# Kernel optimization log

Hardware: AMD Instinct MI355X
Metric: run time of the kernel (lower is better)

The kernel has to match this reference:

```python
import jax, jax.numpy as jnp
import numpy as np
import math

B, S, D, H = 8, 1024, 512, 8
DH = D // H
SCALE_BASE = 512


def _xpos(x, downscale):
    # x: [B, H, S, DH]; xpos rotary with exponential scale (jamie-stirling RetNet impl)
    s = x.shape[-2]
    d = x.shape[-1]
    half = d // 2
    sv = (jnp.arange(0, d, 2, dtype=jnp.float32) + 0.4 * d) / (1.4 * d)      # [half]
    power = jnp.arange(s, dtype=jnp.float32) / SCALE_BASE
    scale = sv[None, :] ** power[:, None]                                     # [s, half]
    inv_freq = 1.0 / (10000.0 ** (jnp.arange(half, dtype=jnp.float32) / half))
    ang = jnp.arange(s, dtype=jnp.float32)[:, None] * inv_freq[None, :]       # [s, half]
    if downscale:
        scale = 1.0 / scale
    sin = jnp.repeat(jnp.sin(ang) * scale, 2, axis=-1)                        # [s, d]
    cos = jnp.repeat(jnp.cos(ang) * scale, 2, axis=-1)
    rot = jnp.stack((-x[..., 1::2], x[..., ::2]), axis=-1).reshape(x.shape)   # rotate_every_two
    return x * cos + rot * sin


def setup_inputs() -> dict:
    key = jax.random.key(0)
    ks = jax.random.split(key, 7)
    X = jax.random.normal(ks[0], (B, S, D), dtype=jnp.float32)
    # per-head projections stacked: torch init randn/hidden_size
    W_Q = jax.random.normal(ks[1], (H, D, DH), dtype=jnp.float32) / D
    W_K = jax.random.normal(ks[2], (H, D, DH), dtype=jnp.float32) / D
    W_V = jax.random.normal(ks[3], (H, D, DH), dtype=jnp.float32) / D
    W_G = jax.random.normal(ks[4], (D, D), dtype=jnp.float32) / D
    W_O = jax.random.normal(ks[5], (D, D), dtype=jnp.float32) / D
    gn_weight = jnp.ones((D,), dtype=jnp.float32)
    gn_bias = jnp.zeros((D,), dtype=jnp.float32)
    return {"X": X, "W_Q": W_Q, "W_K": W_K, "W_V": W_V, "W_G": W_G,
            "W_O": W_O, "gn_weight": gn_weight, "gn_bias": gn_bias}


def reference(X, W_Q, W_K, W_V, W_G, W_O, gn_weight, gn_bias):
    b, s, _ = X.shape
    # per-head decay gammas and symmetric (non-causal) decay matrix D
    gammas = 1.0 - jnp.exp(jnp.linspace(math.log(1.0 / 32), math.log(1.0 / 512), H)).astype(jnp.float32)
    n = jnp.arange(s)
    Dmat = gammas[:, None, None] ** jnp.abs(n[:, None] - n[None, :]).astype(jnp.float32)  # [H,s,s]
    Q = _xpos(jnp.einsum('bsd,hde->bhse', X, W_Q), False)
    K = _xpos(jnp.einsum('bsd,hde->bhse', X, W_K), True)
    V = jnp.einsum('bsd,hde->bhse', X, W_V)
    scores = jnp.einsum('bhse,bhte->bhst', Q, K)
    p = jax.nn.softmax(scores, axis=-1) * Dmat[None]          # decay-weighted softmax
    Y = jnp.einsum('bhst,bhte->bhse', p, V)                    # [b,H,s,DH]
    Y = jnp.moveaxis(Y, 1, 2).reshape(b, s, H * DH)            # concat heads -> [b,s,D]
    # GroupNorm(H groups) over flattened rows [b*s, D]
    Yg = Y.reshape(-1, H, DH)
    mu = Yg.mean(axis=-1, keepdims=True)
    var = Yg.var(axis=-1, keepdims=True)
    Yn = ((Yg - mu) * jax.lax.rsqrt(var + 1e-5)).reshape(-1, H * DH)
    Yn = (Yn * gn_weight + gn_bias).reshape(b, s, H * DH)
    G = X @ W_G
    swish = G * jax.nn.sigmoid(G)
    return (swish * Yn) @ W_O
```

## Files before the change

### kernel.cpp

```cpp
#include <hip/hip_runtime.h>
#include <math.h>

#define B_ 8
#define S_ 1024
#define D_ 512
#define H_ 8
#define DH_ 64
#define M_ (B_*S_)

typedef __attribute__((ext_vector_type(8))) short short8;
typedef __attribute__((ext_vector_type(4))) short s16x4;
typedef __attribute__((ext_vector_type(4))) float f32x4;

__device__ inline unsigned short bf16h(float x) {
  unsigned u = __float_as_uint(x);
  return (unsigned short)((u + 0x7FFFu + ((u >> 16) & 1u)) >> 16);
}
__device__ inline void tsplit(float x, short& hs, short& ls) {
  unsigned u = __float_as_uint(x);
  hs = (short)(u >> 16);
  float r = x - __uint_as_float(u & 0xFFFF0000u);
  ls = (short)(__float_as_uint(r) >> 16);
}
__device__ inline f32x4 mfma16(short8 a, short8 b, f32x4 c) {
  return __builtin_amdgcn_mfma_f32_16x16x32_bf16(a, b, c, 0, 0, 0);
}

__global__ void xpos_table_kernel(float* __restrict__ tab) {
  int idx = blockIdx.x * 256 + threadIdx.x;
  int s = idx >> 5, i = idx & 31;
  float sv = (2.0f * (float)i + 0.4f * 64.0f) / (1.4f * 64.0f);
  float p = (float)s / 512.0f;
  float scale = powf(sv, p);
  float inv_freq = powf(10000.0f, -((float)i / 32.0f));
  float ang = (float)s * inv_freq;
  float sn = sinf(ang), cs = cosf(ang);
  tab[idx]          = cs * scale;
  tab[32768 + idx]  = sn * scale;
  tab[65536 + idx]  = cs / scale;
  tab[98304 + idx]  = sn / scale;
}

__global__ __launch_bounds__(256) void wprep_kernel(
    const float* __restrict__ Wq, const float* __restrict__ Wk,
    const float* __restrict__ Wv, const float* __restrict__ Wg,
    short* __restrict__ BTh, short* __restrict__ BTl, int gonly) {
  __shared__ float t[64][65];
  const int n0 = blockIdx.x * 64, k0 = blockIdx.y * 64;
  const int tid = threadIdx.x;
  const float* src;
  int ld;
  if (gonly) {
    src = Wg + (size_t)k0 * 512 + n0; ld = 512;
  } else {
    int w = n0 >> 9, nn = n0 & 511;
    if (w == 3) { src = Wg + (size_t)k0 * 512 + nn; ld = 512; }
    else {
      const float* W = (w == 0) ? Wq : ((w == 1) ? Wk : Wv);
      int h = nn >> 6;
      src = W + (size_t)h * D_ * DH_ + (size_t)k0 * 64; ld = 64;
    }
  }
#pragma unroll
  for (int i = 0; i < 4; ++i) {
    int idx = tid + i * 256;
    int kk = idx >> 4, nl4 = (idx & 15) * 4;
    float4 v = *(const float4*)(src + (size_t)kk * ld + nl4);
    t[kk][nl4] = v.x; t[kk][nl4 + 1] = v.y; t[kk][nl4 + 2] = v.z; t[kk][nl4 + 3] = v.w;
  }
  __syncthreads();
#pragma unroll
  for (int i = 0; i < 2; ++i) {
    int idx = tid + i * 256;
    int nl = idx >> 3, ck = idx & 7;
    short8 hh, ll;
#pragma unroll
    for (int j = 0; j < 8; ++j) {
      short h_, l_;
      tsplit(t[ck * 8 + j][nl], h_, l_);
      hh[j] = h_; ll[j] = l_;
    }
    size_t off = (size_t)(n0 + nl) * 512 + k0 + ck * 8;
    *(short8*)(BTh + off) = hh;
    *(short8*)(BTl + off) = ll;
  }
}

template<bool PRESPLIT>
__global__ __launch_bounds__(256) void gemm_mfma_kernel(
    const float* __restrict__ Af,
    const short* __restrict__ Ah, const short* __restrict__ Al,
    const short* __restrict__ BTh, const short* __restrict__ BTl,
    float* __restrict__ Qo, float* __restrict__ Ko,
    short* __restrict__ VhT, short* __restrict__ VlT,
    float* __restrict__ G, int fused) {
  __shared__ __align__(16) short AsH[128][40];
  __shared__ __align__(16) short AsL[128][40];
  __shared__ __align__(16) short BsH[128][40];
  __shared__ __align__(16) short BsL[128][40];
  const int m0 = blockIdx.x * 128, by = blockIdx.y, n0 = by * 128;
  const int tid = threadIdx.x, w = tid >> 6, lane = tid & 63;
  const int lx = lane & 15, quad = lane >> 4;
  const int wr = w >> 1, wc = w & 1;
  f32x4 acc[4][4] = {};
  for (int k0 = 0; k0 < 512; k0 += 32) {
    if constexpr (PRESPLIT) {
#pragma unroll
      for (int i = 0; i < 2; ++i) {
        int idx = tid + i * 256;
        int r = idx >> 2, sg = (idx & 3) * 8;
        *(short8*)&AsH[r][sg] = *(const short8*)(Ah + (size_t)(m0 + r) * 512 + k0 + sg);
        *(short8*)&AsL[r][sg] = *(const short8*)(Al + (size_t)(m0 + r) * 512 + k0 + sg);
      }
    } else {
      int r = tid >> 1, kh = (tid & 1) * 16;
      const float* ap = Af + (size_t)(m0 + r) * 512 + k0 + kh;
#pragma unroll
      for (int j4 = 0; j4 < 4; ++j4) {
        float4 v = *(const float4*)(ap + j4 * 4);
        s16x4 hh, ll;
        short h_, l_;
        tsplit(v.x, h_, l_); hh[0] = h_; ll[0] = l_;
        tsplit(v.y, h_, l_); hh[1] = h_; ll[1] = l_;
        tsplit(v.z, h_, l_); hh[2] = h_; ll[2] = l_;
        tsplit(v.w, h_, l_); hh[3] = h_; ll[3] = l_;
        *(s16x4*)&AsH[r][kh + j4 * 4] = hh;
        *(s16x4*)&AsL[r][kh + j4 * 4] = ll;
      }
    }
#pragma unroll
    for (int i = 0; i < 2; ++i) {
      int idx = tid + i * 256;
      int r = idx >> 2, sg = (idx & 3) * 8;
      *(short8*)&BsH[r][sg] = *(const short8*)(BTh + (size_t)(n0 + r) * 512 + k0 + sg);
      *(short8*)&BsL[r][sg] = *(const short8*)(BTl + (size_t)(n0 + r) * 512 + k0 + sg);
    }
    __syncthreads();
    short8 fah[4], fal[4], fbh[4], fbl[4];
#pragma unroll
    for (int i = 0; i < 4; ++i) {
      fah[i] = *(const short8*)&AsH[wr * 64 + i * 16 + lx][quad * 8];
      fal[i] = *(const short8*)&AsL[wr * 64 + i * 16 + lx][quad * 8];
      fbh[i] = *(const short8*)&BsH[wc * 64 + i * 16 + lx][quad * 8];
      fbl[i] = *(const short8*)&BsL[wc * 64 + i * 16 + lx][quad * 8];
    }
#pragma unroll
    for (int ms = 0; ms < 4; ++ms)
#pragma unroll
      for (int ns = 0; ns < 4; ++ns) {
        f32x4 a = acc[ms][ns];
        a = mfma16(fah[ms], fbh[ns], a);
        a = mfma16(fal[ms], fbh[ns], a);
        a = mfma16(fah[ms], fbl[ns], a);
        acc[ms][ns] = a;
      }
    __syncthreads();
  }
  if (fused) {
    const int w4 = by >> 2;
    const int ncb = (by & 3) * 128 + wc * 64;
    if (w4 < 2) {
      float* P = (w4 == 0) ? Qo : Ko;
#pragma unroll
      for (int ms = 0; ms < 4; ++ms) {
        const int m = m0 + wr * 64 + ms * 16 + quad * 4;
        const int b = m >> 10, s = m & 1023;
#pragma unroll
        for (int ns = 0; ns < 4; ++ns) {
          const int n = ncb + ns * 16 + lx;
          const int h = n >> 6, e = n & 63;
          float* bp = P + (((size_t)(b * 8 + h)) * 1024 + s) * 64 + e;
#pragma unroll
          for (int rg = 0; rg < 4; ++rg) bp[rg * 64] = acc[ms][ns][rg];
        }
      }
    } else if (w4 == 2) {
#pragma unroll
      for (int ms = 0; ms < 4; ++ms) {
        const int m = m0 + wr * 64 + ms * 16 + quad * 4;
        const int b = m >> 10, s = m & 1023;
#pragma unroll
        for (int ns = 0; ns < 4; ++ns) {
          const int n = ncb + ns * 16 + lx;
          const int h = n >> 6, e = n & 63;
          s16x4 hh, ll;
#pragma unroll
          for (int rg = 0; rg < 4; ++rg) {
            short h_, l_;
            tsplit(acc[ms][ns][rg], h_, l_);
            hh[rg] = h_; ll[rg] = l_;
          }
          size_t off = (((size_t)(b * 8 + h)) * 64 + e) * 1024 + s;
          *(s16x4*)(VhT + off) = hh;
          *(s16x4*)(VlT + off) = ll;
        }
      }
    } else {
#pragma unroll
      for (int ms = 0; ms < 4; ++ms) {
        const int m = m0 + wr * 64 + ms * 16 + quad * 4;
#pragma unroll
        for (int ns = 0; ns < 4; ++ns) {
          const int n = ncb + ns * 16 + lx;
#pragma unroll
          for (int rg = 0; rg < 4; ++rg) G[(size_t)(m + rg) * 512 + n] = acc[ms][ns][rg];
        }
      }
    }
  } else {
#pragma unroll
    for (int ms = 0; ms < 4; ++ms) {
      const int m = m0 + wr * 64 + ms * 16 + quad * 4;
#pragma unroll
      for (int ns = 0; ns < 4; ++ns) {
        const int n = n0 + wc * 64 + ns * 16 + lx;
#pragma unroll
        for (int rg = 0; rg < 4; ++rg) G[(size_t)(m + rg) * 512 + n] = acc[ms][ns][rg];
      }
    }
  }
}

__global__ __launch_bounds__(256) void rotary_ew_kernel(const float* __restrict__ in,
                                                        float* __restrict__ outp,
                                                        const float* __restrict__ tab, int isK) {
  int idx = blockIdx.x * 256 + threadIdx.x;
  size_t base = (size_t)idx * 4;
  int e4 = (int)(base & 63);
  int s = (int)((base >> 6) & (S_ - 1));
  const float* ct = tab + (isK ? 65536 : 0) + s * 32;
  const float* st = tab + (isK ? 98304 : 32768) + s * 32;
  float4 v = *(const float4*)(in + base);
  int i0 = e4 >> 1;
  float c0 = ct[i0], s0v = st[i0], c1 = ct[i0 + 1], s1v = st[i0 + 1];
  float4 o;
  o.x = v.x * c0 - v.y * s0v;
  o.y = v.y * c0 + v.x * s0v;
  o.z = v.z * c1 - v.w * s1v;
  o.w = v.w * c1 + v.z * s1v;
  *(float4*)(outp + base) = o;
}

__global__ __launch_bounds__(256, 2) void attn_mfma_kernel(const float* __restrict__ Q,
                                                           const float* __restrict__ K,
                                                           const short* __restrict__ VhT,
                                                           const short* __restrict__ VlT,
                                                           float* __restrict__ Y) {
  __shared__ __align__(16) short KhS[64][72];
  __shared__ __align__(16) short KlS[64][72];
  __shared__ __align__(16) short VhS[64][72];
  __shared__ __align__(16) short VlS[64][72];
  __shared__ __align__(16) short PhS[4][32][72];
  const int s0 = blockIdx.x * 128, bh = blockIdx.y;
  const int b = bh >> 3, h = bh & 7;
  const int tid = threadIdx.x;
  const int w = tid >> 6, lane = tid & 63;
  const int lx = lane & 15, quad = lane >> 4;
  const int s0w = s0 + w * 32;
  const float l0c = -3.4657359027997265f;
  const float l1c = -6.2383246250395075f;
  const float gamma = 1.0f - expf(l0c + (float)h * (l1c - l0c) / 7.0f);
  const float lg2g = log2f(gamma);
  const float* Qb = Q + (size_t)bh * S_ * DH_;
  const float* Kb = K + (size_t)bh * S_ * DH_;
  const short* VbH = VhT + (size_t)bh * DH_ * S_;
  const short* VbL = VlT + (size_t)bh * DH_ * S_;

  float cl[4], cr[4];
#pragma unroll
  for (int ns = 0; ns < 4; ++ns) {
    cl[ns] = exp2f(lg2g * (float)(ns * 16 + lx));
    cr[ns] = exp2f(lg2g * (float)(63 - ns * 16 - lx));
  }

  short8 qh[2][2], ql[2][2];
#pragma unroll
  for (int ms = 0; ms < 2; ++ms)
#pragma unroll
    for (int kc = 0; kc < 2; ++kc) {
      const float* qp = Qb + (size_t)(s0w + ms * 16 + lx) * DH_ + kc * 32 + quad * 8;
      float4 a = *(const float4*)qp, c = *(const float4*)(qp + 4);
      float xs[8] = {a.x, a.y, a.z, a.w, c.x, c.y, c.z, c.w};
      short8 hh, ll;
#pragma unroll
      for (int j = 0; j < 8; ++j) {
        short h_, l_;
        tsplit(xs[j], h_, l_);
        hh[j] = h_; ll[j] = l_;
      }
      qh[ms][kc] = hh; ql[ms][kc] = ll;
    }

  f32x4 O[2][4] = {};
  float lsum[2][4] = {};

  for (int t0 = 0; t0 < S_; t0 += 64) {
    __syncthreads();
#pragma unroll
    for (int i = 0; i < 4; ++i) {
      int r = (tid >> 4) + i * 16, c4 = (tid & 15) * 4;
      float4 kv = *(const float4*)(Kb + (size_t)(t0 + r) * DH_ + c4);
      float ks[4] = {kv.x, kv.y, kv.z, kv.w};
      s16x4 h4, l4;
#pragma unroll
      for (int j = 0; j < 4; ++j) {
        short h_, l_;
        tsplit(ks[j], h_, l_);
        h4[j] = h_; l4[j] = l_;
      }
      *(s16x4*)&KhS[r][c4] = h4;
      *(s16x4*)&KlS[r][c4] = l4;
    }
#pragma unroll
    for (int i = 0; i < 2; ++i) {
      int idx = tid + i * 256;
      int e = idx >> 3, c8 = (idx & 7) * 8;
      *(short8*)&VhS[e][c8] = *(const short8*)(VbH + (size_t)e * S_ + t0 + c8);
      *(short8*)&VlS[e][c8] = *(const short8*)(VbL + (size_t)e * S_ + t0 + c8);
    }
    __syncthreads();
    f32x4 acc[2][4];
#pragma unroll
    for (int ns = 0; ns < 4; ++ns) {
      short8 kh0 = *(const short8*)&KhS[ns * 16 + lx][quad * 8];
      short8 kh1 = *(const short8*)&KhS[ns * 16 + lx][32 + quad * 8];
      short8 kl0 = *(const short8*)&KlS[ns * 16 + lx][quad * 8];
      short8 kl1 = *(const short8*)&KlS[ns * 16 + lx][32 + quad * 8];
#pragma unroll
      for (int ms = 0; ms < 2; ++ms) {
        f32x4 a = {};
        a = mfma16(qh[ms][0], kh0, a);
        a = mfma16(ql[ms][0], kh0, a);
        a = mfma16(qh[ms][0], kl0, a);
        a = mfma16(qh[ms][1], kh1, a);
        a = mfma16(ql[ms][1], kh1, a);
        a = mfma16(qh[ms][1], kl1, a);
        acc[ms][ns] = a;
      }
    }
    const int cse = (t0 + 63 < s0w) ? 0 : ((t0 > s0w + 31) ? 1 : 2);
#pragma unroll
    for (int ms = 0; ms < 2; ++ms)
#pragma unroll
      for (int rg = 0; rg < 4; ++rg) {
        const int rloc = ms * 16 + quad * 4 + rg;
        const int srow = s0w + rloc;
        float pe[4], p[4];
#pragma unroll
        for (int ns = 0; ns < 4; ++ns) pe[ns] = __expf(acc[ms][ns][rg]);
        lsum[ms][rg] += (pe[0] + pe[1]) + (pe[2] + pe[3]);
        if (cse == 0) {
          float rf = exp2f(lg2g * (float)(srow - t0 - 63));
#pragma unroll
          for (int ns = 0; ns < 4; ++ns) p[ns] = pe[ns] * rf * cr[ns];
        } else if (cse == 1) {
          float rf = exp2f(lg2g * (float)(t0 - srow));
#pragma unroll
          for (int ns = 0; ns < 4; ++ns) p[ns] = pe[ns] * rf * cl[ns];
        } else {
#pragma unroll
          for (int ns = 0; ns < 4; ++ns)
            p[ns] = pe[ns] * exp2f(lg2g * fabsf((float)(srow - (t0 + ns * 16 + lx))));
        }
#pragma unroll
        for (int ns = 0; ns < 4; ++ns)
          PhS[w][rloc][ns * 16 + lx] = (short)bf16h(p[ns]);
      }
    short8 pf[2][2];
#pragma unroll
    for (int ms = 0; ms < 2; ++ms)
#pragma unroll
      for (int kc = 0; kc < 2; ++kc)
        pf[ms][kc] = *(const short8*)&PhS[w][ms * 16 + lx][kc * 32 + quad * 8];
#pragma unroll
    for (int ns = 0; ns < 4; ++ns) {
      short8 vh0 = *(const short8*)&VhS[ns * 16 + lx][quad * 8];
      short8 vh1 = *(const short8*)&VhS[ns * 16 + lx][32 + quad * 8];
      short8 vl0 = *(const short8*)&VlS[ns * 16 + lx][quad * 8];
      short8 vl1 = *(const short8*)&VlS[ns * 16 + lx][32 + quad * 8];
#pragma unroll
      for (int ms = 0; ms < 2; ++ms) {
        f32x4 o = O[ms][ns];
        o = mfma16(pf[ms][0], vh0, o);
        o = mfma16(pf[ms][0], vl0, o);
        o = mfma16(pf[ms][1], vh1, o);
        o = mfma16(pf[ms][1], vl1, o);
        O[ms][ns] = o;
      }
    }
  }
#pragma unroll
  for (int ms = 0; ms < 2; ++ms)
#pragma unroll
    for (int rg = 0; rg < 4; ++rg) {
      float s = lsum[ms][rg];
      s += __shfl_xor(s, 1);
      s += __shfl_xor(s, 2);
      s += __shfl_xor(s, 4);
      s += __shfl_xor(s, 8);
      const float inv = 1.0f / s;
      const int srow = s0w + ms * 16 + quad * 4 + rg;
#pragma unroll
      for (int ns = 0; ns < 4; ++ns)
        Y[((size_t)(b * S_ + srow)) * D_ + h * DH_ + ns * 16 + lx] = O[ms][ns][rg] * inv;
    }
}

__global__ __launch_bounds__(256) void gn_gate_kernel(const float* __restrict__ Y,
                                                      const float* __restrict__ G,
                                                      const float* __restrict__ gnw,
                                                      const float* __restrict__ gnb,
                                                      short* __restrict__ Zh,
                                                      short* __restrict__ Zl) {
  const int r0 = blockIdx.x * 64, h = blockIdx.y, d0 = h * DH_;
  const int tid = threadIdx.x, tx = tid & 15, tyq = tid >> 4;
  float4 wv = *(const float4*)(gnw + d0 + tx * 4);
  float4 bv = *(const float4*)(gnb + d0 + tx * 4);
  float w4[4] = {wv.x, wv.y, wv.z, wv.w};
  float b4[4] = {bv.x, bv.y, bv.z, bv.w};
#pragma unroll
  for (int i = 0; i < 4; ++i) {
    int r = r0 + tyq + i * 16;
    float4 yv = *(const float4*)(Y + (size_t)r * D_ + d0 + tx * 4);
    float y[4] = {yv.x, yv.y, yv.z, yv.w};
    float s = y[0] + y[1] + y[2] + y[3];
    s += __shfl_xor(s, 1); s += __shfl_xor(s, 2); s += __shfl_xor(s, 4); s += __shfl_xor(s, 8);
    const float mu = s * (1.0f / 64.0f);
    float d0_ = y[0] - mu, d1 = y[1] - mu, d2 = y[2] - mu, d3 = y[3] - mu;
    float ss = d0_ * d0_ + d1 * d1 + d2 * d2 + d3 * d3;
    ss += __shfl_xor(ss, 1); ss += __shfl_xor(ss, 2); ss += __shfl_xor(ss, 4); ss += __shfl_xor(ss, 8);
    const float rstd = 1.0f / sqrtf(ss * (1.0f / 64.0f) + 1e-5f);
    float4 gv = *(const float4*)(G + (size_t)r * D_ + d0 + tx * 4);
    float g[4] = {gv.x, gv.y, gv.z, gv.w};
    s16x4 hh, ll;
#pragma unroll
    for (int j = 0; j < 4; ++j) {
      float yn = (y[j] - mu) * rstd * w4[j] + b4[j];
      float sw = g[j] / (1.0f + expf(-g[j]));
      short h_, l_;
      tsplit(sw * yn, h_, l_);
      hh[j] = h_; ll[j] = l_;
    }
    size_t off = (size_t)r * 512 + d0 + tx * 4;
    *(s16x4*)(Zh + off) = hh;
    *(s16x4*)(Zl + off) = ll;
  }
}

extern "C" void kernel_launch(void* const* d_in, const int* in_sizes, int n_in,
                              void* d_out, int out_size, void* d_ws, size_t ws_size,
                              hipStream_t stream) {
  const float* X   = (const float*)d_in[0];
  const float* Wq  = (const float*)d_in[1];
  const float* Wk  = (const float*)d_in[2];
  const float* Wv  = (const float*)d_in[3];
  const float* Wg  = (const float*)d_in[4];
  const float* Wo  = (const float*)d_in[5];
  const float* gnw = (const float*)d_in[6];
  const float* gnb = (const float*)d_in[7];
  float* out = (float*)d_out;
  float* ws  = (float*)d_ws;
  const size_t NB = (size_t)M_ * D_;
  float* R0 = ws;
  float* R1 = ws + NB;
  float* R2 = ws + 2 * NB;
  float* R3 = ws + 3 * NB;
  float* tab = ws + 4 * NB;
  short* BTh = (short*)R3;
  short* BTl = BTh + (size_t)2048 * 512;
  short* VhT = (short*)R2;
  short* VlT = VhT + (size_t)64 * 64 * 1024 / 64 * DH_;
  short* Zh = (short*)R0;
  short* Zl = Zh + (size_t)M_ * 512;
  short* BToh = (short*)R1;
  short* BTol = BToh + (size_t)512 * 512;

  wprep_kernel<<<dim3(32, 8), 256, 0, stream>>>(Wq, Wk, Wv, Wg, BTh, BTl, 0);
  xpos_table_kernel<<<128, 256, 0, stream>>>(tab);
  gemm_mfma_kernel<false><<<dim3(64, 16), 256, 0, stream>>>(
      X, nullptr, nullptr, BTh, BTl, R0, R1, VhT, VlT, out, 1);
  rotary_ew_kernel<<<4096, 256, 0, stream>>>(R0, R3, tab, 0);
  rotary_ew_kernel<<<4096, 256, 0, stream>>>(R1, R0, tab, 1);
  attn_mfma_kernel<<<dim3(8, 64), 256, 0, stream>>>(R3, R0, VhT, VlT, R1);
  gn_gate_kernel<<<dim3(128, 8), 256, 0, stream>>>(R1, out, gnw, gnb, Zh, Zl);
  wprep_kernel<<<dim3(8, 8), 256, 0, stream>>>(nullptr, nullptr, nullptr, Wo, BToh, BTol, 1);
  gemm_mfma_kernel<true><<<dim3(64, 4), 256, 0, stream>>>(
      nullptr, Zh, Zl, BToh, BTol, nullptr, nullptr, nullptr, nullptr, out, 0);
}
```

Before: 257.3 us.

## Fuse xpos rotary and bf16 split into QKV GEMM epilogue

The xpos rotary is now applied in the projection GEMM epilogue, using a lane shuffle to fetch the paired element. Q and K are written as presplit bf16 hi/lo arrays instead of fp32, which removes both rotary elementwise kernels and the per-tile splitting of K and Q inside attention. Attention now loads K tiles directly as short8 vectors. Its grid is transposed so consecutive blocks share the same batch-head, which may improve L2 reuse. The epilogue now does scattered 2-byte stores and table loads, and workspace buffers are reassigned.

```diff
diff --git a/kernel.cpp b/kernel.cpp
--- a/kernel.cpp
+++ b/kernel.cpp
@@ -91,7 +91,9 @@
     const float* __restrict__ Af,
     const short* __restrict__ Ah, const short* __restrict__ Al,
     const short* __restrict__ BTh, const short* __restrict__ BTl,
-    float* __restrict__ Qo, float* __restrict__ Ko,
+    const float* __restrict__ tab,
+    short* __restrict__ QhO, short* __restrict__ QlO,
+    short* __restrict__ KhO, short* __restrict__ KlO,
     short* __restrict__ VhT, short* __restrict__ VlT,
     float* __restrict__ G, int fused) {
   __shared__ __align__(16) short AsH[128][40];
@@ -160,18 +162,33 @@
     const int w4 = by >> 2;
     const int ncb = (by & 3) * 128 + wc * 64;
     if (w4 < 2) {
-      float* P = (w4 == 0) ? Qo : Ko;
+      short* Ph = (w4 == 0) ? QhO : KhO;
+      short* Pl = (w4 == 0) ? QlO : KlO;
+      const float* ct = tab + (w4 ? 65536 : 0);
+      const float* st = tab + (w4 ? 98304 : 32768);
 #pragma unroll
       for (int ms = 0; ms < 4; ++ms) {
         const int m = m0 + wr * 64 + ms * 16 + quad * 4;
-        const int b = m >> 10, s = m & 1023;
+        const int b = m >> 10, sbase = m & 1023;
 #pragma unroll
         for (int ns = 0; ns < 4; ++ns) {
           const int n = ncb + ns * 16 + lx;
           const int h = n >> 6, e = n & 63;
-          float* bp = P + (((size_t)(b * 8 + h)) * 1024 + s) * 64 + e;
-#pragma unroll
-          for (int rg = 0; rg < 4; ++rg) bp[rg * 64] = acc[ms][ns][rg];
+          const int i0 = e >> 1;
+          const float sgn = (e & 1) ? 1.0f : -1.0f;
+          short* ph = Ph + (((size_t)(b * 8 + h)) * 1024 + sbase) * 64 + e;
+          short* pl = Pl + (((size_t)(b * 8 + h)) * 1024 + sbase) * 64 + e;
+#pragma unroll
+          for (int rg = 0; rg < 4; ++rg) {
+            const int s = sbase + rg;
+            float v = acc[ms][ns][rg];
+            float vp = __shfl_xor(v, 1);
+            float o = v * ct[s * 32 + i0] + sgn * vp * st[s * 32 + i0];
+            short h_, l_;
+            tsplit(o, h_, l_);
+            ph[rg * 64] = h_;
+            pl[rg * 64] = l_;
+          }
         }
       }
     } else if (w4 == 2) {
@@ -221,37 +238,17 @@
   }
 }
 
-__global__ __launch_bounds__(256) void rotary_ew_kernel(const float* __restrict__ in,
-                                                        float* __restrict__ outp,
-                                                        const float* __restrict__ tab, int isK) {
-  int idx = blockIdx.x * 256 + threadIdx.x;
-  size_t base = (size_t)idx * 4;
-  int e4 = (int)(base & 63);
-  int s = (int)((base >> 6) & (S_ - 1));
-  const float* ct = tab + (isK ? 65536 : 0) + s * 32;
-  const float* st = tab + (isK ? 98304 : 32768) + s * 32;
-  float4 v = *(const float4*)(in + base);
-  int i0 = e4 >> 1;
-  float c0 = ct[i0], s0v = st[i0], c1 = ct[i0 + 1], s1v = st[i0 + 1];
-  float4 o;
-  o.x = v.x * c0 - v.y * s0v;
-  o.y = v.y * c0 + v.x * s0v;
-  o.z = v.z * c1 - v.w * s1v;
-  o.w = v.w * c1 + v.z * s1v;
-  *(float4*)(outp + base) = o;
-}
-
-__global__ __launch_bounds__(256, 2) void attn_mfma_kernel(const float* __restrict__ Q,
-                                                           const float* __restrict__ K,
-                                                           const short* __restrict__ VhT,
-                                                           const short* __restrict__ VlT,
-                                                           float* __restrict__ Y) {
+__global__ __launch_bounds__(256, 2) void attn_mfma_kernel(
+    const short* __restrict__ Qh, const short* __restrict__ Ql,
+    const short* __restrict__ Kh, const short* __restrict__ Kl,
+    const short* __restrict__ VhT, const short* __restrict__ VlT,
+    float* __restrict__ Y) {
   __shared__ __align__(16) short KhS[64][72];
   __shared__ __align__(16) short KlS[64][72];
   __shared__ __align__(16) short VhS[64][72];
   __shared__ __align__(16) short VlS[64][72];
   __shared__ __align__(16) short PhS[4][32][72];
-  const int s0 = blockIdx.x * 128, bh = blockIdx.y;
+  const int bh = blockIdx.x, s0 = blockIdx.y * 128;
   const int b = bh >> 3, h = bh & 7;
   const int tid = threadIdx.x;
   const int w = tid >> 6, lane = tid & 63;
@@ -261,8 +258,10 @@
   const float l1c = -6.2383246250395075f;
   const float gamma = 1.0f - expf(l0c + (float)h * (l1c - l0c) / 7.0f);
   const float lg2g = log2f(gamma);
-  const float* Qb = Q + (size_t)bh * S_ * DH_;
-  const float* Kb = K + (size_t)bh * S_ * DH_;
+  const short* Qbh = Qh + (size_t)bh * S_ * DH_;
+  const short* Qbl = Ql + (size_t)bh * S_ * DH_;
+  const short* Kbh = Kh + (size_t)bh * S_ * DH_;
+  const short* Kbl = Kl + (size_t)bh * S_ * DH_;
   const short* VbH = VhT + (size_t)bh * DH_ * S_;
   const short* VbL = VlT + (size_t)bh * DH_ * S_;
 
@@ -273,22 +272,14 @@
     cr[ns] = exp2f(lg2g * (float)(63 - ns * 16 - lx));
   }
 
-  short8 qh[2][2], ql[2][2];
+  short8 qfh[2][2], qfl[2][2];
 #pragma unroll
   for (int ms = 0; ms < 2; ++ms)
 #pragma unroll
     for (int kc = 0; kc < 2; ++kc) {
-      const float* qp = Qb + (size_t)(s0w + ms * 16 + lx) * DH_ + kc * 32 + quad * 8;
-      float4 a = *(const float4*)qp, c = *(const float4*)(qp + 4);
-      float xs[8] = {a.x, a.y, a.z, a.w, c.x, c.y, c.z, c.w};
-      short8 hh, ll;
-#pragma unroll
-      for (int j = 0; j < 8; ++j) {
-        short h_, l_;
-        tsplit(xs[j], h_, l_);
-        hh[j] = h_; ll[j] = l_;
-      }
-      qh[ms][kc] = hh; ql[ms][kc] = ll;
+      size_t off = (size_t)(s0w + ms * 16 + lx) * DH_ + kc * 32 + quad * 8;
+      qfh[ms][kc] = *(const short8*)(Qbh + off);
+      qfl[ms][kc] = *(const short8*)(Qbl + off);
     }
 
   f32x4 O[2][4] = {};
@@ -297,26 +288,13 @@
   for (int t0 = 0; t0 < S_; t0 += 64) {
     __syncthreads();
 #pragma unroll
-    for (int i = 0; i < 4; ++i) {
-      int r = (tid >> 4) + i * 16, c4 = (tid & 15) * 4;
-      float4 kv = *(const float4*)(Kb + (size_t)(t0 + r) * DH_ + c4);
-      float ks[4] = {kv.x, kv.y, kv.z, kv.w};
-      s16x4 h4, l4;
-#pragma unroll
-      for (int j = 0; j < 4; ++j) {
-        short h_, l_;
-        tsplit(ks[j], h_, l_);
-        h4[j] = h_; l4[j] = l_;
-      }
-      *(s16x4*)&KhS[r][c4] = h4;
-      *(s16x4*)&KlS[r][c4] = l4;
-    }
-#pragma unroll
     for (int i = 0; i < 2; ++i) {
-      int idx = tid + i * 256;
-      int e = idx >> 3, c8 = (idx & 7) * 8;
-      *(short8*)&VhS[e][c8] = *(const short8*)(VbH + (size_t)e * S_ + t0 + c8);
-      *(short8*)&VlS[e][c8] = *(const short8*)(VbL + (size_t)e * S_ + t0 + c8);
+      int slot = tid + i * 256;
+      int r = slot >> 3, c8 = (slot & 7) * 8;
+      *(short8*)&KhS[r][c8] = *(const short8*)(Kbh + (size_t)(t0 + r) * DH_ + c8);
+      *(short8*)&KlS[r][c8] = *(const short8*)(Kbl + (size_t)(t0 + r) * DH_ + c8);
+      *(short8*)&VhS[r][c8] = *(const short8*)(VbH + (size_t)r * S_ + t0 + c8);
+      *(short8*)&VlS[r][c8] = *(const short8*)(VbL + (size_t)r * S_ + t0 + c8);
     }
     __syncthreads();
     f32x4 acc[2][4];
@@ -329,12 +307,12 @@
 #pragma unroll
       for (int ms = 0; ms < 2; ++ms) {
         f32x4 a = {};
-        a = mfma16(qh[ms][0], kh0, a);
-        a = mfma16(ql[ms][0], kh0, a);
-        a = mfma16(qh[ms][0], kl0, a);
-        a = mfma16(qh[ms][1], kh1, a);
-        a = mfma16(ql[ms][1], kh1, a);
-        a = mfma16(qh[ms][1], kl1, a);
+        a = mfma16(qfh[ms][0], kh0, a);
+        a = mfma16(qfl[ms][0], kh0, a);
+        a = mfma16(qfh[ms][0], kl0, a);
+        a = mfma16(qfh[ms][1], kh1, a);
+        a = mfma16(qfl[ms][1], kh1, a);
+        a = mfma16(qfh[ms][1], kl1, a);
         acc[ms][ns] = a;
       }
     }
@@ -468,22 +446,22 @@
   float* tab = ws + 4 * NB;
   short* BTh = (short*)R3;
   short* BTl = BTh + (size_t)2048 * 512;
-  short* VhT = (short*)R2;
-  short* VlT = VhT + (size_t)64 * 64 * 1024 / 64 * DH_;
-  short* Zh = (short*)R0;
-  short* Zl = Zh + (size_t)M_ * 512;
+  short* Qh = (short*)R0;  short* Ql = Qh + NB;
+  short* Kh = (short*)R1;  short* Kl = Kh + NB;
+  short* VhT = (short*)R2; short* VlT = VhT + NB;
+  float* Yb = R3;
+  short* Zh = (short*)R0;  short* Zl = Zh + NB;
   short* BToh = (short*)R1;
   short* BTol = BToh + (size_t)512 * 512;
 
   wprep_kernel<<<dim3(32, 8), 256, 0, stream>>>(Wq, Wk, Wv, Wg, BTh, BTl, 0);
   xpos_table_kernel<<<128, 256, 0, stream>>>(tab);
   gemm_mfma_kernel<false><<<dim3(64, 16), 256, 0, stream>>>(
-      X, nullptr, nullptr, BTh, BTl, R0, R1, VhT, VlT, out, 1);
-  rotary_ew_kernel<<<4096, 256, 0, stream>>>(R0, R3, tab, 0);
-  rotary_ew_kernel<<<4096, 256, 0, stream>>>(R1, R0, tab, 1);
-  attn_mfma_kernel<<<dim3(8, 64), 256, 0, stream>>>(R3, R0, VhT, VlT, R1);
-  gn_gate_kernel<<<dim3(128, 8), 256, 0, stream>>>(R1, out, gnw, gnb, Zh, Zl);
+      X, nullptr, nullptr, BTh, BTl, tab, Qh, Ql, Kh, Kl, VhT, VlT, out, 1);
+  attn_mfma_kernel<<<dim3(64, 8), 256, 0, stream>>>(Qh, Ql, Kh, Kl, VhT, VlT, Yb);
+  gn_gate_kernel<<<dim3(128, 8), 256, 0, stream>>>(Yb, out, gnw, gnb, Zh, Zl);
   wprep_kernel<<<dim3(8, 8), 256, 0, stream>>>(nullptr, nullptr, nullptr, Wo, BToh, BTol, 1);
   gemm_mfma_kernel<true><<<dim3(64, 4), 256, 0, stream>>>(
-      nullptr, Zh, Zl, BToh, BTol, nullptr, nullptr, nullptr, nullptr, out, 0);
-}
+      nullptr, Zh, Zl, BToh, BTol, nullptr, nullptr, nullptr, nullptr, nullptr,
+      nullptr, nullptr, out, 0);
+}
```

Result: faster. 241.9 us (-6.0%).
